# Kernel tuning notes

Measured on AMD Instinct MI355X. Metric: run time of the kernel, lower is better.

Reference implementation:

```python
import jax, jax.numpy as jnp
import numpy as np

D_MODEL = 256
NHEAD = 8
HEAD_DIM = D_MODEL // NHEAD
LN_EPS = 1e-5
NEG_INF = -1e30  # finite large-negative; avoids NaN rows while matching masked softmax


def setup_inputs() -> dict:
    key = jax.random.key(0)
    ks = jax.random.split(key, 9)
    B, Q, HW, D = 8, 100, 16384, D_MODEL
    s = 0.02
    return {
        "query": jax.random.normal(ks[0], (B, Q, D), jnp.float32),
        "key_value": jax.random.normal(ks[1], (B, HW, D), jnp.float32),
        "attn_mask": jax.random.randint(ks[2], (B * NHEAD, Q, HW), 0, 2) == 1,  # True = attend
        "in_proj_weight": jax.random.normal(ks[3], (3 * D, D), jnp.float32) * s,
        "in_proj_bias": jax.random.normal(ks[4], (3 * D,), jnp.float32) * s,
        "out_proj_weight": jax.random.normal(ks[5], (D, D), jnp.float32) * s,
        "out_proj_bias": jax.random.normal(ks[6], (D,), jnp.float32) * s,
        "ln_weight": jnp.ones((D,), jnp.float32),
        "ln_bias": jnp.zeros((D,), jnp.float32),
    }


def _mha_masked(query, key_value, attn_mask, in_proj_weight, in_proj_bias,
                out_proj_weight, out_proj_bias):
    B, Q, D = query.shape
    HW = key_value.shape[1]
    Wq, Wk, Wv = jnp.split(in_proj_weight, 3, axis=0)
    bq, bk, bv = jnp.split(in_proj_bias, 3, axis=0)
    q = (query @ Wq.T + bq).reshape(B, Q, NHEAD, HEAD_DIM)
    k = (key_value @ Wk.T + bk).reshape(B, HW, NHEAD, HEAD_DIM)
    v = (key_value @ Wv.T + bv).reshape(B, HW, NHEAD, HEAD_DIM)
    scale = 1.0 / np.sqrt(HEAD_DIM).astype(np.float32)
    scores = jnp.einsum("bqhd,bkhd->bhqk", q, k) * scale  # (B, H, Q, HW)
    attend = attn_mask.reshape(B, NHEAD, Q, HW)  # True = attend
    scores = jnp.where(attend, scores, NEG_INF)
    probs = jax.nn.softmax(scores, axis=-1)
    ctx = jnp.einsum("bhqk,bkhd->bqhd", probs, v).reshape(B, Q, D)
    return ctx @ out_proj_weight.T + out_proj_bias


def reference(query, key_value, attn_mask, in_proj_weight, in_proj_bias,
              out_proj_weight, out_proj_bias, ln_weight, ln_bias):
    attn_out = _mha_masked(query, key_value, attn_mask, in_proj_weight,
                           in_proj_bias, out_proj_weight, out_proj_bias)
    x = query + attn_out  # dropout p=0.0 is identity
    mu = jnp.mean(x, axis=-1, keepdims=True)
    var = jnp.mean(jnp.square(x - mu), axis=-1, keepdims=True)
    return (x - mu) * jax.lax.rsqrt(var + LN_EPS) * ln_weight + ln_bias
```

## Files before the change

kernel.cpp:

```cpp
#include <hip/hip_runtime.h>
#include <stdint.h>

#define BB   8
#define NH   8
#define QQ   100
#define HWK  16384
#define DM   256
#define HD   32
#define QP   112
#define MT   7
#define NPART 64
#define SCALE2 0.2550602534365564f

typedef short bf16x8 __attribute__((ext_vector_type(8)));
typedef float f32x4  __attribute__((ext_vector_type(4)));
typedef unsigned short u16;
typedef unsigned int   u32;
typedef unsigned long long u64;

__device__ __forceinline__ u16 f2bf(float f) {
  u32 u = __builtin_bit_cast(u32, f);
  u += 0x7fffu + ((u >> 16) & 1u);
  return (u16)(u >> 16);
}
__device__ __forceinline__ u16 f2bf_ru(float f) {
  return (u16)((__builtin_bit_cast(u32, f) + 0x8000u) >> 16);
}
__device__ __forceinline__ u32 pack2rn(float lo, float hi) {
  u32 a = __builtin_bit_cast(u32, lo) + 0x8000u;
  u32 b = __builtin_bit_cast(u32, hi) + 0x8000u;
  return __builtin_amdgcn_perm(b, a, 0x07060302u);
}
__device__ __forceinline__ float fast_exp2(float x) {
#if __has_builtin(__builtin_amdgcn_exp2f)
  return __builtin_amdgcn_exp2f(x);
#else
  return exp2f(x);
#endif
}

__global__ __launch_bounds__(256) void wconv_kernel(
    const float* __restrict__ W, u16* __restrict__ wbf) {
  const int i = (blockIdx.x * 256 + threadIdx.x) * 4;
  const float4 w = *(const float4*)(W + 256 * DM + i);
  u32* dst = (u32*)(wbf + i);
  dst[0] = pack2rn(w.x, w.y);
  dst[1] = pack2rn(w.z, w.w);
}

__global__ __launch_bounds__(256) void proj_q_kernel(
    const float* __restrict__ query, const float* __restrict__ W,
    const float* __restrict__ bias, u16* __restrict__ q_bf) {
  __shared__ float xrow[DM];
  const int bq = blockIdx.x;
  const int b = bq / QQ, qi = bq % QQ;
  const int tid = threadIdx.x;
  if (tid < 64)
    ((float4*)xrow)[tid] = ((const float4*)(query + (size_t)bq * DM))[tid];
  __syncthreads();
  const int j = tid;
  float acc = bias[j];
  const float4* wr = (const float4*)(W + (size_t)j * DM);
  #pragma unroll 8
  for (int c = 0; c < 64; ++c) {
    float4 w = wr[c];
    float4 x = ((const float4*)xrow)[c];
    acc += w.x * x.x + w.y * x.y + w.z * x.z + w.w * x.w;
  }
  acc *= SCALE2;
  const int h = j >> 5, d = j & 31;
  q_bf[(((size_t)(b * NH + h)) * QQ + qi) * HD + d] = f2bf(acc);
}

__global__ __launch_bounds__(256) void proj_kv_kernel(
    const float* __restrict__ kv, const u16* __restrict__ wbf,
    const float* __restrict__ bias, u16* __restrict__ k_bf,
    u16* __restrict__ v_t) {
  __shared__ u16 Tl[4][5120];
  const int rb = blockIdx.x;
  const size_t m0 = (size_t)rb * 64;
  const int tid = threadIdx.x, lane = tid & 63, wid = tid >> 6;
  const int lane15 = lane & 15, quad = lane >> 4;
  const int jw = wid * 128;

  f32x4 acc[4][8];
  #pragma unroll
  for (int mi = 0; mi < 4; ++mi)
    #pragma unroll
    for (int ni = 0; ni < 8; ++ni) acc[mi][ni] = (f32x4){0.f, 0.f, 0.f, 0.f};

  for (int ks = 0; ks < 8; ++ks) {
    bf16x8 afr[4];
    #pragma unroll
    for (int mi = 0; mi < 4; ++mi) {
      const float* ap = kv + (m0 + mi * 16 + lane15) * DM + ks * 32 + quad * 8;
      float4 a0 = ((const float4*)ap)[0];
      float4 a1 = ((const float4*)ap)[1];
      uint4 w;
      w.x = pack2rn(a0.x, a0.y); w.y = pack2rn(a0.z, a0.w);
      w.z = pack2rn(a1.x, a1.y); w.w = pack2rn(a1.z, a1.w);
      afr[mi] = __builtin_bit_cast(bf16x8, w);
    }
    #pragma unroll
    for (int ni = 0; ni < 8; ++ni) {
      bf16x8 bfr = __builtin_bit_cast(bf16x8,
          *(const uint4*)(wbf + (size_t)(jw + ni * 16 + lane15) * DM + ks * 32 + quad * 8));
      #pragma unroll
      for (int mi = 0; mi < 4; ++mi)
        acc[mi][ni] = __builtin_amdgcn_mfma_f32_16x16x32_bf16(afr[mi], bfr, acc[mi][ni], 0, 0, 0);
    }
  }

  u16* T = Tl[wid];
  const float* bptr = bias + 256 + jw;
  if (wid < 2) {
    #pragma unroll
    for (int p = 0; p < 2; ++p) {
      #pragma unroll
      for (int mm = 0; mm < 2; ++mm) {
        const int mi = p * 2 + mm;
        #pragma unroll
        for (int ni = 0; ni < 8; ++ni) {
          const float bv = bptr[ni * 16 + lane15];
          #pragma unroll
          for (int r = 0; r < 4; ++r)
            T[(mm * 16 + quad * 4 + r) * 136 + ni * 16 + lane15] =
                f2bf_ru(acc[mi][ni][r] + bv);
        }
      }
      #pragma unroll
      for (int it = 0; it < 8; ++it) {
        const int row = it * 4 + quad;
        const int c0 = lane15 * 8;
        uint4 val = *(const uint4*)&T[row * 136 + c0];
        const size_t m = m0 + p * 32 + row;
        const size_t b = m >> 14, key = m & 16383;
        const int col256 = jw + c0;
        const int h = col256 >> 5, d = col256 & 31;
        *(uint4*)&k_bf[((b * NH + h) * HWK + key) * HD + d] = val;
      }
    }
  } else {
    const int jwv = jw - 256;
    #pragma unroll
    for (int p = 0; p < 2; ++p) {
      #pragma unroll
      for (int mm = 0; mm < 2; ++mm) {
        const int mi = p * 2 + mm;
        #pragma unroll
        for (int ni = 0; ni < 8; ++ni) {
          const float bv = bptr[ni * 16 + lane15];
          u32* dst = (u32*)&T[(ni * 16 + lane15) * 40 + mm * 16 + quad * 4];
          dst[0] = pack2rn(acc[mi][ni][0] + bv, acc[mi][ni][1] + bv);
          dst[1] = pack2rn(acc[mi][ni][2] + bv, acc[mi][ni][3] + bv);
        }
      }
      #pragma unroll
      for (int it = 0; it < 8; ++it) {
        const int col = it * 16 + (lane >> 2);
        const int koff = (lane & 3) * 8;
        uint4 val = *(const uint4*)&T[col * 40 + koff];
        const size_t m = m0 + p * 32 + koff;
        const size_t b = m >> 14, key = m & 16383;
        const int col256 = jwv + col;
        const int h = col256 >> 5, d = col256 & 31;
        *(uint4*)&v_t[((b * NH + h) * HD + d) * HWK + key] = val;
      }
    }
  }
}

__global__ __launch_bounds__(256) void attn_kernel(
    const u16* __restrict__ q_bf, const u16* __restrict__ k_bf,
    const u16* __restrict__ v_t, const int* __restrict__ mask,
    float* __restrict__ l_p, float* __restrict__ ctx_p) {
  __shared__ u16 qlds[QP * 40];
  __shared__ u64 mbits[QQ][16];
  __shared__ float plds[4][16 * 36];
  const int tid = threadIdx.x;
  const int lane = tid & 63, wid = tid >> 6;
  const int lane15 = lane & 15, quad = lane >> 4;
  const int bh = blockIdx.x >> 4, chunk = blockIdx.x & 15;

  for (int i = tid; i < QP * HD; i += 256) {
    const int row = i >> 5, d = i & 31;
    qlds[row * 40 + d] = (row < QQ) ? q_bf[((size_t)bh * QQ + row) * HD + d] : (u16)0;
  }
  {
    const int* mp_base = mask + (size_t)bh * QQ * HWK + chunk * 1024;
    for (int rr = 0; rr < 25; ++rr) {
      const int row = wid * 25 + rr;
      const int* mp = mp_base + (size_t)row * HWK;
      u64 mine = 0;
      #pragma unroll
      for (int g = 0; g < 16; ++g) {
        const int mv = mp[g * 64 + lane];
        const u64 bl = __ballot(mv != 0);
        if (lane == g) mine = bl;
      }
      if (lane < 16) mbits[row][lane] = mine;
    }
  }
  __syncthreads();
  const u32* mw = (const u32*)mbits;

  const int klocal_base = wid * 256;
  const int key_base = chunk * 1024 + klocal_base;
  const u16* kbase = k_bf + (size_t)bh * HWK * HD;
  const u16* vtb  = v_t  + (size_t)bh * HWK * HD;

  f32x4 acc[MT][2];
  float l_run[MT][4];
  #pragma unroll
  for (int mt = 0; mt < MT; ++mt) {
    acc[mt][0] = (f32x4){0.f, 0.f, 0.f, 0.f};
    acc[mt][1] = (f32x4){0.f, 0.f, 0.f, 0.f};
    #pragma unroll
    for (int r = 0; r < 4; ++r) l_run[mt][r] = 0.f;
  }
  float* pl = plds[wid];

  for (int kg = 0; kg < 8; ++kg) {
    const int key0 = key_base + kg * 32;
    const int widx = (klocal_base + kg * 32) >> 5;
    bf16x8 kf0 = __builtin_bit_cast(bf16x8,
        *(const uint4*)(kbase + (size_t)(key0 + lane15) * HD + quad * 8));
    bf16x8 kf1 = __builtin_bit_cast(bf16x8,
        *(const uint4*)(kbase + (size_t)(key0 + 16 + lane15) * HD + quad * 8));
    bf16x8 vf0 = __builtin_bit_cast(bf16x8,
        *(const uint4*)(vtb + (size_t)lane15 * HWK + key0 + quad * 8));
    bf16x8 vf1 = __builtin_bit_cast(bf16x8,
        *(const uint4*)(vtb + (size_t)(lane15 + 16) * HWK + key0 + quad * 8));
    #pragma unroll
    for (int mt = 0; mt < MT; ++mt) {
      bf16x8 af = __builtin_bit_cast(bf16x8,
          *(const uint4*)&qlds[(mt * 16 + lane15) * 40 + quad * 8]);
      const f32x4 zero = {0.f, 0.f, 0.f, 0.f};
      f32x4 s0 = __builtin_amdgcn_mfma_f32_16x16x32_bf16(af, kf0, zero, 0, 0, 0);
      f32x4 s1 = __builtin_amdgcn_mfma_f32_16x16x32_bf16(af, kf1, zero, 0, 0, 0);
      #pragma unroll
      for (int r = 0; r < 4; ++r) {
        const int rowg = mt * 16 + quad * 4 + r;
        const u32 word = (rowg < QQ) ? mw[rowg * 32 + widx] : 0u;
        const float p0 = ((word >> lane15) & 1u) ? fast_exp2(s0[r]) : 0.f;
        const float p1 = ((word >> (lane15 + 16)) & 1u) ? fast_exp2(s1[r]) : 0.f;
        l_run[mt][r] += p0 + p1;
        pl[(quad * 4 + r) * 36 + lane15]      = p0;
        pl[(quad * 4 + r) * 36 + lane15 + 16] = p1;
      }
      float4 f0 = *(const float4*)&pl[lane15 * 36 + quad * 8];
      float4 f1 = *(const float4*)&pl[lane15 * 36 + quad * 8 + 4];
      uint4 pw;
      pw.x = pack2rn(f0.x, f0.y); pw.y = pack2rn(f0.z, f0.w);
      pw.z = pack2rn(f1.x, f1.y); pw.w = pack2rn(f1.z, f1.w);
      bf16x8 pf = __builtin_bit_cast(bf16x8, pw);
      acc[mt][0] = __builtin_amdgcn_mfma_f32_16x16x32_bf16(pf, vf0, acc[mt][0], 0, 0, 0);
      acc[mt][1] = __builtin_amdgcn_mfma_f32_16x16x32_bf16(pf, vf1, acc[mt][1], 0, 0, 0);
    }
  }

  const int part = chunk * 4 + wid;
  #pragma unroll
  for (int mt = 0; mt < MT; ++mt) {
    #pragma unroll
    for (int r = 0; r < 4; ++r) {
      const int row = mt * 16 + quad * 4 + r;
      float lr = l_run[mt][r];
      lr += __shfl_xor(lr, 1);
      lr += __shfl_xor(lr, 2);
      lr += __shfl_xor(lr, 4);
      lr += __shfl_xor(lr, 8);
      const size_t base = ((size_t)bh * QP + row) * NPART + part;
      if (lane15 == 0) l_p[base] = lr;
      ctx_p[base * HD + lane15]      = acc[mt][0][r];
      ctx_p[base * HD + lane15 + 16] = acc[mt][1][r];
    }
  }
}

__global__ __launch_bounds__(256) void combine_kernel(
    const float* __restrict__ l_p, const float* __restrict__ ctx_p,
    const float* __restrict__ query, const float* __restrict__ Wo,
    const float* __restrict__ bo, const float* __restrict__ lnw,
    const float* __restrict__ lnb, float* __restrict__ out) {
  __shared__ float ctx_row[DM];
  __shared__ float red[8];
  const int bq = blockIdx.x;
  const int b = bq / QQ, qi = bq % QQ;
  const int tid = threadIdx.x, lane = tid & 63, wid = tid >> 6;

  for (int hh = 0; hh < 2; ++hh) {
    const int h = wid * 2 + hh;
    const size_t base = ((size_t)(b * NH + h) * QP + qi) * NPART;
    float lv = l_p[base + lane];
    #pragma unroll
    for (int o = 1; o < 64; o <<= 1) lv += __shfl_xor(lv, o);
    const float inv_l = 1.0f / lv;
    const int d4 = (lane & 7) * 4, pg = lane >> 3;
    float4 s4 = {0.f, 0.f, 0.f, 0.f};
    for (int p = pg; p < NPART; p += 8) {
      float4 c = *(const float4*)(ctx_p + (base + p) * HD + d4);
      s4.x += c.x; s4.y += c.y; s4.z += c.z; s4.w += c.w;
    }
    #pragma unroll
    for (int o = 8; o < 64; o <<= 1) {
      s4.x += __shfl_xor(s4.x, o);
      s4.y += __shfl_xor(s4.y, o);
      s4.z += __shfl_xor(s4.z, o);
      s4.w += __shfl_xor(s4.w, o);
    }
    if (pg == 0) {
      ctx_row[h * HD + d4]     = s4.x * inv_l;
      ctx_row[h * HD + d4 + 1] = s4.y * inv_l;
      ctx_row[h * HD + d4 + 2] = s4.z * inv_l;
      ctx_row[h * HD + d4 + 3] = s4.w * inv_l;
    }
  }
  __syncthreads();

  const int j = tid;
  float s = bo[j];
  const float4* wr = (const float4*)(Wo + (size_t)j * DM);
  #pragma unroll 8
  for (int c = 0; c < 64; ++c) {
    float4 wv = wr[c];
    float4 cx = ((const float4*)ctx_row)[c];
    s += wv.x * cx.x + wv.y * cx.y + wv.z * cx.z + wv.w * cx.w;
  }
  const float x = s + query[(size_t)bq * DM + j];

  float t = x;
  #pragma unroll
  for (int o = 1; o < 64; o <<= 1) t += __shfl_xor(t, o);
  if (lane == 0) red[wid] = t;
  __syncthreads();
  const float mu = (red[0] + red[1] + red[2] + red[3]) * (1.0f / DM);
  const float dx = x - mu;
  float t2 = dx * dx;
  #pragma unroll
  for (int o = 1; o < 64; o <<= 1) t2 += __shfl_xor(t2, o);
  if (lane == 0) red[4 + wid] = t2;
  __syncthreads();
  const float var = (red[4] + red[5] + red[6] + red[7]) * (1.0f / DM);
  out[(size_t)bq * DM + j] = dx * rsqrtf(var + 1e-5f) * lnw[j] + lnb[j];
}

extern "C" void kernel_launch(void* const* d_in, const int* in_sizes, int n_in,
                              void* d_out, int out_size, void* d_ws, size_t ws_size,
                              hipStream_t stream) {
  const float* query = (const float*)d_in[0];
  const float* kv    = (const float*)d_in[1];
  const int*   mask  = (const int*)d_in[2];
  const float* ipw   = (const float*)d_in[3];
  const float* ipb   = (const float*)d_in[4];
  const float* opw   = (const float*)d_in[5];
  const float* opb   = (const float*)d_in[6];
  const float* lnw   = (const float*)d_in[7];
  const float* lnb   = (const float*)d_in[8];
  float* out = (float*)d_out;

  char* ws = (char*)d_ws;
  u16*   k_bf  = (u16*)(ws);
  u16*   v_t   = (u16*)(ws + 67108864);
  u16*   q_bf  = (u16*)(ws + 134217728);
  float* l_p   = (float*)(ws + 134742016);
  float* ctx_p = (float*)(ws + 136577024);
  u16*   wbf   = (u16*)(ws + 195297280);

  wconv_kernel  <<<128,          256, 0, stream>>>(ipw, wbf);
  proj_q_kernel <<<BB * QQ,      256, 0, stream>>>(query, ipw, ipb, q_bf);
  proj_kv_kernel<<<2048,         256, 0, stream>>>(kv, wbf, ipb, k_bf, v_t);
  attn_kernel   <<<BB * NH * 16, 256, 0, stream>>>(q_bf, k_bf, v_t, mask, l_p, ctx_p);
  combine_kernel<<<BB * QQ,      256, 0, stream>>>(l_p, ctx_p, query, opw, opb, lnw, lnb, out);
}
```

Baseline: 878.8 us.

## Transpose score MFMA and pass probabilities via shuffles; store partial ctx in bf16

New measurement: 868.4 us. No clear change (-1.2%).

```diff
diff --git a/kernel.cpp b/kernel.cpp
--- a/kernel.cpp
+++ b/kernel.cpp
@@ -31,6 +31,12 @@
   u32 b = __builtin_bit_cast(u32, hi) + 0x8000u;
   return __builtin_amdgcn_perm(b, a, 0x07060302u);
 }
+__device__ __forceinline__ float bf_lo(u32 u) {
+  return __builtin_bit_cast(float, u << 16);
+}
+__device__ __forceinline__ float bf_hi(u32 u) {
+  return __builtin_bit_cast(float, u & 0xffff0000u);
+}
 __device__ __forceinline__ float fast_exp2(float x) {
 #if __has_builtin(__builtin_amdgcn_exp2f)
   return __builtin_amdgcn_exp2f(x);
@@ -173,10 +179,9 @@
 __global__ __launch_bounds__(256) void attn_kernel(
     const u16* __restrict__ q_bf, const u16* __restrict__ k_bf,
     const u16* __restrict__ v_t, const int* __restrict__ mask,
-    float* __restrict__ l_p, float* __restrict__ ctx_p) {
+    float* __restrict__ l_p, u32* __restrict__ ctxp) {
   __shared__ u16 qlds[QP * 40];
-  __shared__ u64 mbits[QQ][16];
-  __shared__ float plds[4][16 * 36];
+  __shared__ u32 mbitsw[QP * 33];
   const int tid = threadIdx.x;
   const int lane = tid & 63, wid = tid >> 6;
   const int lane15 = lane & 15, quad = lane >> 4;
@@ -191,38 +196,40 @@
     for (int rr = 0; rr < 25; ++rr) {
       const int row = wid * 25 + rr;
       const int* mp = mp_base + (size_t)row * HWK;
-      u64 mine = 0;
+      u32 myw = 0;
       #pragma unroll
       for (int g = 0; g < 16; ++g) {
         const int mv = mp[g * 64 + lane];
         const u64 bl = __ballot(mv != 0);
-        if (lane == g) mine = bl;
-      }
-      if (lane < 16) mbits[row][lane] = mine;
-    }
-  }
-  __syncthreads();
-  const u32* mw = (const u32*)mbits;
+        if (lane == 2 * g)     myw = (u32)bl;
+        if (lane == 2 * g + 1) myw = (u32)(bl >> 32);
+      }
+      if (lane < 32) mbitsw[row * 33 + lane] = myw;
+    }
+  }
+  __syncthreads();
 
   const int klocal_base = wid * 256;
   const int key_base = chunk * 1024 + klocal_base;
   const u16* kbase = k_bf + (size_t)bh * HWK * HD;
   const u16* vtb  = v_t  + (size_t)bh * HWK * HD;
 
+  const int sl_lo = lane15 + 32 * (quad & 1);
+  const int sl_hi = sl_lo + 16;
+  const u32 selperm = (quad & 2) ? 0x07060302u : 0x05040100u;
+
   f32x4 acc[MT][2];
-  float l_run[MT][4];
+  float l_run[MT];
   #pragma unroll
   for (int mt = 0; mt < MT; ++mt) {
     acc[mt][0] = (f32x4){0.f, 0.f, 0.f, 0.f};
     acc[mt][1] = (f32x4){0.f, 0.f, 0.f, 0.f};
-    #pragma unroll
-    for (int r = 0; r < 4; ++r) l_run[mt][r] = 0.f;
-  }
-  float* pl = plds[wid];
+    l_run[mt] = 0.f;
+  }
 
   for (int kg = 0; kg < 8; ++kg) {
     const int key0 = key_base + kg * 32;
-    const int widx = (klocal_base + kg * 32) >> 5;
+    const int widx = wid * 8 + kg;
     bf16x8 kf0 = __builtin_bit_cast(bf16x8,
         *(const uint4*)(kbase + (size_t)(key0 + lane15) * HD + quad * 8));
     bf16x8 kf1 = __builtin_bit_cast(bf16x8,
@@ -233,53 +240,65 @@
         *(const uint4*)(vtb + (size_t)(lane15 + 16) * HWK + key0 + quad * 8));
     #pragma unroll
     for (int mt = 0; mt < MT; ++mt) {
+      const int rowg = mt * 16 + lane15;
       bf16x8 af = __builtin_bit_cast(bf16x8,
-          *(const uint4*)&qlds[(mt * 16 + lane15) * 40 + quad * 8]);
+          *(const uint4*)&qlds[rowg * 40 + quad * 8]);
       const f32x4 zero = {0.f, 0.f, 0.f, 0.f};
-      f32x4 s0 = __builtin_amdgcn_mfma_f32_16x16x32_bf16(af, kf0, zero, 0, 0, 0);
-      f32x4 s1 = __builtin_amdgcn_mfma_f32_16x16x32_bf16(af, kf1, zero, 0, 0, 0);
+      f32x4 s0 = __builtin_amdgcn_mfma_f32_16x16x32_bf16(kf0, af, zero, 0, 0, 0);
+      f32x4 s1 = __builtin_amdgcn_mfma_f32_16x16x32_bf16(kf1, af, zero, 0, 0, 0);
+      u32 word = mbitsw[rowg * 33 + widx];
+      if (rowg >= QQ) word = 0u;
+      u32 pk[4];
+      float lsum = 0.f;
       #pragma unroll
       for (int r = 0; r < 4; ++r) {
-        const int rowg = mt * 16 + quad * 4 + r;
-        const u32 word = (rowg < QQ) ? mw[rowg * 32 + widx] : 0u;
-        const float p0 = ((word >> lane15) & 1u) ? fast_exp2(s0[r]) : 0.f;
-        const float p1 = ((word >> (lane15 + 16)) & 1u) ? fast_exp2(s1[r]) : 0.f;
-        l_run[mt][r] += p0 + p1;
-        pl[(quad * 4 + r) * 36 + lane15]      = p0;
-        pl[(quad * 4 + r) * 36 + lane15 + 16] = p1;
-      }
-      float4 f0 = *(const float4*)&pl[lane15 * 36 + quad * 8];
-      float4 f1 = *(const float4*)&pl[lane15 * 36 + quad * 8 + 4];
+        const int kl = quad * 4 + r;
+        const float p0 = ((word >> kl) & 1u)        ? fast_exp2(s0[r]) : 0.f;
+        const float p1 = ((word >> (kl + 16)) & 1u) ? fast_exp2(s1[r]) : 0.f;
+        lsum += p0 + p1;
+        pk[r] = pack2rn(p0, p1);
+      }
+      l_run[mt] += lsum;
+      u32 wA0 = (u32)__shfl((int)pk[0], sl_lo);
+      u32 wA1 = (u32)__shfl((int)pk[1], sl_lo);
+      u32 wA2 = (u32)__shfl((int)pk[2], sl_lo);
+      u32 wA3 = (u32)__shfl((int)pk[3], sl_lo);
+      u32 wB0 = (u32)__shfl((int)pk[0], sl_hi);
+      u32 wB1 = (u32)__shfl((int)pk[1], sl_hi);
+      u32 wB2 = (u32)__shfl((int)pk[2], sl_hi);
+      u32 wB3 = (u32)__shfl((int)pk[3], sl_hi);
       uint4 pw;
-      pw.x = pack2rn(f0.x, f0.y); pw.y = pack2rn(f0.z, f0.w);
-      pw.z = pack2rn(f1.x, f1.y); pw.w = pack2rn(f1.z, f1.w);
+      pw.x = __builtin_amdgcn_perm(wA1, wA0, selperm);
+      pw.y = __builtin_amdgcn_perm(wA3, wA2, selperm);
+      pw.z = __builtin_amdgcn_perm(wB1, wB0, selperm);
+      pw.w = __builtin_amdgcn_perm(wB3, wB2, selperm);
       bf16x8 pf = __builtin_bit_cast(bf16x8, pw);
-      acc[mt][0] = __builtin_amdgcn_mfma_f32_16x16x32_bf16(pf, vf0, acc[mt][0], 0, 0, 0);
-      acc[mt][1] = __builtin_amdgcn_mfma_f32_16x16x32_bf16(pf, vf1, acc[mt][1], 0, 0, 0);
+      acc[mt][0] = __builtin_amdgcn_mfma_f32_16x16x32_bf16(vf0, pf, acc[mt][0], 0, 0, 0);
+      acc[mt][1] = __builtin_amdgcn_mfma_f32_16x16x32_bf16(vf1, pf, acc[mt][1], 0, 0, 0);
     }
   }
 
   const int part = chunk * 4 + wid;
   #pragma unroll
   for (int mt = 0; mt < MT; ++mt) {
-    #pragma unroll
-    for (int r = 0; r < 4; ++r) {
-      const int row = mt * 16 + quad * 4 + r;
-      float lr = l_run[mt][r];
-      lr += __shfl_xor(lr, 1);
-      lr += __shfl_xor(lr, 2);
-      lr += __shfl_xor(lr, 4);
-      lr += __shfl_xor(lr, 8);
-      const size_t base = ((size_t)bh * QP + row) * NPART + part;
-      if (lane15 == 0) l_p[base] = lr;
-      ctx_p[base * HD + lane15]      = acc[mt][0][r];
-      ctx_p[base * HD + lane15 + 16] = acc[mt][1][r];
-    }
+    const int row = mt * 16 + lane15;
+    float lr = l_run[mt];
+    lr += __shfl_xor(lr, 16);
+    lr += __shfl_xor(lr, 32);
+    const size_t base = ((size_t)bh * QP + row) * NPART + part;
+    if (quad == 0) l_p[base] = lr;
+    uint2 lo2, hi2;
+    lo2.x = pack2rn(acc[mt][0][0], acc[mt][0][1]);
+    lo2.y = pack2rn(acc[mt][0][2], acc[mt][0][3]);
+    hi2.x = pack2rn(acc[mt][1][0], acc[mt][1][1]);
+    hi2.y = pack2rn(acc[mt][1][2], acc[mt][1][3]);
+    *(uint2*)&ctxp[base * 16 + quad * 2]     = lo2;
+    *(uint2*)&ctxp[base * 16 + 8 + quad * 2] = hi2;
   }
 }
 
 __global__ __launch_bounds__(256) void combine_kernel(
-    const float* __restrict__ l_p, const float* __restrict__ ctx_p,
+    const float* __restrict__ l_p, const u32* __restrict__ ctxp,
     const float* __restrict__ query, const float* __restrict__ Wo,
     const float* __restrict__ bo, const float* __restrict__ lnw,
     const float* __restrict__ lnb, float* __restrict__ out) {
@@ -296,24 +315,26 @@
     #pragma unroll
     for (int o = 1; o < 64; o <<= 1) lv += __shfl_xor(lv, o);
     const float inv_l = 1.0f / lv;
-    const int d4 = (lane & 7) * 4, pg = lane >> 3;
-    float4 s4 = {0.f, 0.f, 0.f, 0.f};
+    const int c = lane & 7, pg = lane >> 3;
+    const u32* cp = ctxp + base * 16 + c * 2;
+    float s0 = 0.f, s1 = 0.f, s2 = 0.f, s3 = 0.f;
     for (int p = pg; p < NPART; p += 8) {
-      float4 c = *(const float4*)(ctx_p + (base + p) * HD + d4);
-      s4.x += c.x; s4.y += c.y; s4.z += c.z; s4.w += c.w;
+      uint2 u = *(const uint2*)(cp + (size_t)p * 16);
+      s0 += bf_lo(u.x); s1 += bf_hi(u.x);
+      s2 += bf_lo(u.y); s3 += bf_hi(u.y);
     }
     #pragma unroll
     for (int o = 8; o < 64; o <<= 1) {
-      s4.x += __shfl_xor(s4.x, o);
-      s4.y += __shfl_xor(s4.y, o);
-      s4.z += __shfl_xor(s4.z, o);
-      s4.w += __shfl_xor(s4.w, o);
+      s0 += __shfl_xor(s0, o);
+      s1 += __shfl_xor(s1, o);
+      s2 += __shfl_xor(s2, o);
+      s3 += __shfl_xor(s3, o);
     }
     if (pg == 0) {
-      ctx_row[h * HD + d4]     = s4.x * inv_l;
-      ctx_row[h * HD + d4 + 1] = s4.y * inv_l;
-      ctx_row[h * HD + d4 + 2] = s4.z * inv_l;
-      ctx_row[h * HD + d4 + 3] = s4.w * inv_l;
+      ctx_row[h * HD + c * 4]     = s0 * inv_l;
+      ctx_row[h * HD + c * 4 + 1] = s1 * inv_l;
+      ctx_row[h * HD + c * 4 + 2] = s2 * inv_l;
+      ctx_row[h * HD + c * 4 + 3] = s3 * inv_l;
     }
   }
   __syncthreads();
@@ -364,12 +385,12 @@
   u16*   v_t   = (u16*)(ws + 67108864);
   u16*   q_bf  = (u16*)(ws + 134217728);
   float* l_p   = (float*)(ws + 134742016);
-  float* ctx_p = (float*)(ws + 136577024);
+  u32*   ctxp  = (u32*)(ws + 136577024);
   u16*   wbf   = (u16*)(ws + 195297280);
 
   wconv_kernel  <<<128,          256, 0, stream>>>(ipw, wbf);
   proj_q_kernel <<<BB * QQ,      256, 0, stream>>>(query, ipw, ipb, q_bf);
   proj_kv_kernel<<<2048,         256, 0, stream>>>(kv, wbf, ipb, k_bf, v_t);
-  attn_kernel   <<<BB * NH * 16, 256, 0, stream>>>(q_bf, k_bf, v_t, mask, l_p, ctx_p);
-  combine_kernel<<<BB * QQ,      256, 0, stream>>>(l_p, ctx_p, query, opw, opb, lnw, lnb, out);
-}
+  attn_kernel   <<<BB * NH * 16, 256, 0, stream>>>(q_bf, k_bf, v_t, mask, l_p, ctxp);
+  combine_kernel<<<BB * QQ,      256, 0, stream>>>(l_p, ctxp, query, opw, opb, lnw, lnb, out);
+}
```
